# Performance work log

Hardware: AMD Instinct MI355X
Metric: run time of the kernel (lower is better)

Reference implementation:

```python
import jax, jax.numpy as jnp
import numpy as np

N, E, NFEAT, HID, HEADS, NCLASS = 100000, 1600000, 256, 64, 1, 32


def gat_conv(x, src, dst, W, a_src, a_dst, b, H, C, concat):
    n = x.shape[0]
    h = (x @ W).reshape(n, H, C)                      # [N,H,C]
    a_s = (h * a_src).sum(-1)                          # [N,H]
    a_d = (h * a_dst).sum(-1)                          # [N,H]
    e = jax.nn.leaky_relu(a_s[src] + a_d[dst], 0.2)    # [E,H]
    emax = jax.ops.segment_max(e, dst, num_segments=n)
    emax = jnp.where(jnp.isfinite(emax), emax, 0.0)
    ex = jnp.exp(e - emax[dst])
    denom = jax.ops.segment_sum(ex, dst, num_segments=n)
    alpha = ex / (denom[dst] + 1e-16)                  # segment softmax over in-edges of dst
    msg = h[src] * alpha[:, :, None]                   # [E,H,C]
    out = jax.ops.segment_sum(msg, dst, num_segments=n)
    out = out.reshape(n, H * C) if concat else out.mean(axis=1)
    return out + b


def setup_inputs() -> dict:
    key = jax.random.key(0)
    ks = jax.random.split(key, 14)
    x = jax.random.normal(ks[0], (N, NFEAT), dtype=jnp.float32)
    edge_index = jax.random.randint(ks[1], (2, E), 0, N, dtype=jnp.int64)
    s = 0.05
    return {
        'x': x, 'edge_index': edge_index,
        'W1': jax.random.normal(ks[2], (NFEAT, HEADS * HID), jnp.float32) * s,
        'as1': jax.random.normal(ks[3], (HEADS, HID), jnp.float32) * s,
        'ad1': jax.random.normal(ks[4], (HEADS, HID), jnp.float32) * s,
        'b1': jnp.zeros((HEADS * HID,), jnp.float32),
        'W2': jax.random.normal(ks[5], (HEADS * HID, HEADS * HID), jnp.float32) * s,
        'as2': jax.random.normal(ks[6], (HEADS, HID), jnp.float32) * s,
        'ad2': jax.random.normal(ks[7], (HEADS, HID), jnp.float32) * s,
        'b2': jnp.zeros((HEADS * HID,), jnp.float32),
        'W3': jax.random.normal(ks[8], (HEADS * HID, HEADS * NCLASS), jnp.float32) * s,
        'as3': jax.random.normal(ks[9], (HEADS, NCLASS), jnp.float32) * s,
        'ad3': jax.random.normal(ks[10], (HEADS, NCLASS), jnp.float32) * s,
        'b3': jnp.zeros((NCLASS,), jnp.float32),
    }


def reference(x, edge_index, W1, as1, ad1, b1, W2, as2, ad2, b2, W3, as3, ad3, b3):
    # add self loops (PyG GATConv add_self_loops=True)
    loop = jnp.arange(N, dtype=edge_index.dtype)
    src = jnp.concatenate([edge_index[0], loop])
    dst = jnp.concatenate([edge_index[1], loop])
    out = jax.nn.leaky_relu(gat_conv(x, src, dst, W1, as1, ad1, b1, HEADS, HID, True), 0.01)
    out = jax.nn.leaky_relu(gat_conv(out, src, dst, W2, as2, ad2, b2, HEADS, HID, True), 0.01)
    out = gat_conv(out, src, dst, W3, as3, ad3, b3, HEADS, NCLASS, False)
    return out
```

## Files before the change

kernel.cpp:

```cpp
#include <hip/hip_runtime.h>

#define NN 100000
#define NE 1600000
#define NF 256
#define HD 64
#define NC 32

#define BKS 8
#define NBK ((NN + 255) >> 8)
#define CHUNK 4096
#define NBLK ((NE + CHUNK - 1) / CHUNK)

__device__ __forceinline__ float lrelu02(float x) { return fmaxf(x, 0.2f * x); }

typedef __attribute__((ext_vector_type(8))) short bf16x8;
typedef __attribute__((ext_vector_type(4))) float f32x4;
typedef __attribute__((ext_vector_type(4))) _Float16 f16x4;

__device__ __forceinline__ unsigned short f2bf(float f) {
    unsigned int u = __float_as_uint(f);
    unsigned int r = u + 0x7FFFu + ((u >> 16) & 1u);
    return (unsigned short)(r >> 16);
}
__device__ __forceinline__ float bf2f(unsigned short s) {
    return __uint_as_float(((unsigned int)s) << 16);
}


__global__ __launch_bounds__(256) void bucket_hist(const int* __restrict__ dst, int* __restrict__ gcnt) {
    __shared__ int hist[NBK];
    int tid = threadIdx.x;
    for (int i = tid; i < NBK; i += 256) hist[i] = 0;
    __syncthreads();
    int base = blockIdx.x * CHUNK;
    #pragma unroll
    for (int k = 0; k < CHUNK / 256; k++) {
        int i = base + k * 256 + tid;
        if (i < NE) atomicAdd(&hist[dst[i] >> BKS], 1);
    }
    __syncthreads();
    for (int i = tid; i < NBK; i += 256) if (hist[i]) atomicAdd(&gcnt[i], hist[i]);
}

__global__ void bucket_scan(const int* __restrict__ gcnt, int* __restrict__ gbase, int* __restrict__ gcur) {
    __shared__ int sh[512];
    int tid = threadIdx.x;
    int v = (tid < NBK) ? gcnt[tid] : 0;
    sh[tid] = v;
    __syncthreads();
    for (int d = 1; d < 512; d <<= 1) {
        int t = (tid >= d) ? sh[tid - d] : 0;
        __syncthreads();
        sh[tid] += t;
        __syncthreads();
    }
    if (tid < NBK) { int ex = sh[tid] - v; gbase[tid] = ex; gcur[tid] = ex; }
}

__global__ __launch_bounds__(256) void bin_edges(const int* __restrict__ src, const int* __restrict__ dst,
                                                 int* __restrict__ gcur, int2* __restrict__ ebuf) {
    __shared__ int hist[NBK];
    __shared__ int excl[NBK];
    __shared__ int runbase[NBK];
    __shared__ int ssum[256];
    __shared__ int2 sorted[CHUNK];
    int tid = threadIdx.x;
    int base = blockIdx.x * CHUNK;
    int n = NE - base; if (n > CHUNK) n = CHUNK;

    for (int i = tid; i < NBK; i += 256) hist[i] = 0;
    __syncthreads();

    int2 ed[CHUNK / 256];
    int bk[CHUNK / 256];
    #pragma unroll
    for (int k = 0; k < CHUNK / 256; k++) {
        int i = base + k * 256 + tid;
        if (i < NE) {
            ed[k] = make_int2(src[i], dst[i]);
            bk[k] = ed[k].y >> BKS;
            atomicAdd(&hist[bk[k]], 1);
        } else bk[k] = -1;
    }
    __syncthreads();
    int h0 = (2 * tid < NBK) ? hist[2 * tid] : 0;
    int h1 = (2 * tid + 1 < NBK) ? hist[2 * tid + 1] : 0;
    ssum[tid] = h0 + h1;
    __syncthreads();
    for (int d = 1; d < 256; d <<= 1) {
        int t = (tid >= d) ? ssum[tid - d] : 0;
        __syncthreads();
        ssum[tid] += t;
        __syncthreads();
    }
    int pref = ssum[tid] - (h0 + h1);
    if (2 * tid < NBK) excl[2 * tid] = pref;
    if (2 * tid + 1 < NBK) excl[2 * tid + 1] = pref + h0;
    for (int b = tid; b < NBK; b += 256) {
        int c = hist[b];
        runbase[b] = c ? atomicAdd(&gcur[b], c) : 0;
    }
    __syncthreads();
    #pragma unroll
    for (int k = 0; k < CHUNK / 256; k++) {
        if (bk[k] >= 0) {
            int r = atomicAdd(&excl[bk[k]], 1);
            sorted[r] = ed[k];
        }
    }
    __syncthreads();
    for (int i = tid; i < n; i += 256) {
        int2 e = sorted[i];
        int b = e.y >> BKS;
        int local_rank = i - (excl[b] - hist[b]);
        ebuf[runbase[b] + local_rank] = e;
    }
}

__global__ __launch_bounds__(256) void bucket_csr(const int2* __restrict__ ebuf, const int* __restrict__ gbase,
                                                  const int* __restrict__ gcnt,
                                                  int* __restrict__ offs, int* __restrict__ csr) {
    __shared__ int hist[256], cur[256], ssum[256];
    int b = blockIdx.x, tid = threadIdx.x;
    int ebeg = gbase[b], cnt = gcnt[b];
    int node0 = b << BKS;
    hist[tid] = 0;
    __syncthreads();
    for (int i = ebeg + tid; i < ebeg + cnt; i += 256)
        atomicAdd(&hist[ebuf[i].y & 255], 1);
    __syncthreads();
    int v = hist[tid];
    ssum[tid] = v;
    __syncthreads();
    for (int d = 1; d < 256; d <<= 1) {
        int t = (tid >= d) ? ssum[tid - d] : 0;
        __syncthreads();
        ssum[tid] += t;
        __syncthreads();
    }
    int ex = ebeg + ssum[tid] - v;
    cur[tid] = ex;
    int nnode = NN - node0; if (nnode > 256) nnode = 256;
    if (tid < nnode) offs[node0 + tid] = ex;
    if (b == NBK - 1 && tid == nnode - 1) offs[NN] = ebeg + cnt;
    __syncthreads();
    for (int i = ebeg + tid; i < ebeg + cnt; i += 256) {
        int2 e = ebuf[i];
        int pos = atomicAdd(&cur[e.y & 255], 1);
        csr[pos] = e.x;
    }
}


template <int CIN, int COUT>
__global__ __launch_bounds__(128) void mfma_gemm(const float* __restrict__ in, const float* __restrict__ W,
                                                 const float* __restrict__ a_s, const float* __restrict__ a_d,
                                                 _Float16* __restrict__ hout, float* __restrict__ asv,
                                                 float* __restrict__ adv) {
    const int KC  = 32;
    const int BM  = 64;
    const int NCT = COUT / 16;
    const int NCH = CIN / KC;
    const int SPT = (4 * COUT) / 128;

    __shared__ unsigned short Bh[2][4 * COUT * 8];
    __shared__ unsigned short Bl[2][4 * COUT * 8];

    int tid  = threadIdx.x;
    int lane = tid & 63;
    int wave = tid >> 6;
    int fr = lane & 15;
    int kg = lane >> 4;
    int n0base = blockIdx.x * BM;
    int rbase  = n0base + wave * 32;

    int scol[SPT], skg[SPT];
    #pragma unroll
    for (int i = 0; i < SPT; i++) {
        int s = tid + i * 128;
        scol[i] = s % COUT;
        skg[i]  = s / COUT;
    }

    float4 xr[4];
    float  wv[SPT][8];
    bf16x8 ah[2], al[2];

    f32x4 acc[2][NCT];
    #pragma unroll
    for (int rt = 0; rt < 2; rt++)
        #pragma unroll
        for (int ct = 0; ct < NCT; ct++) acc[rt][ct] = (f32x4){0.f, 0.f, 0.f, 0.f};

    auto load_A = [&](int k0) {
        #pragma unroll
        for (int rt = 0; rt < 2; rt++) {
            int gr = rbase + rt * 16 + fr;
            if (gr < NN) {
                const float* p = &in[(size_t)gr * CIN + k0 + kg * 8];
                xr[rt * 2 + 0] = *(const float4*)p;
                xr[rt * 2 + 1] = *(const float4*)(p + 4);
            } else {
                xr[rt * 2 + 0] = make_float4(0.f, 0.f, 0.f, 0.f);
                xr[rt * 2 + 1] = make_float4(0.f, 0.f, 0.f, 0.f);
            }
        }
    };
    auto conv_A = [&]() {
        #pragma unroll
        for (int rt = 0; rt < 2; rt++) {
            const float* v = (const float*)&xr[rt * 2];
            unsigned short hs[8], ls[8];
            #pragma unroll
            for (int j = 0; j < 8; j++) {
                hs[j] = f2bf(v[j]);
                ls[j] = f2bf(v[j] - bf2f(hs[j]));
            }
            ah[rt] = *(bf16x8*)hs;
            al[rt] = *(bf16x8*)ls;
        }
    };
    auto load_B = [&](int k0) {
        #pragma unroll
        for (int i = 0; i < SPT; i++)
            #pragma unroll
            for (int j = 0; j < 8; j++)
                wv[i][j] = W[(size_t)(k0 + skg[i] * 8 + j) * COUT + scol[i]];
    };
    auto write_B = [&](int buf) {
        #pragma unroll
        for (int i = 0; i < SPT; i++) {
            unsigned short hs[8], ls[8];
            #pragma unroll
            for (int j = 0; j < 8; j++) {
                hs[j] = f2bf(wv[i][j]);
                ls[j] = f2bf(wv[i][j] - bf2f(hs[j]));
            }
            int idx = (skg[i] * COUT + scol[i]) * 8;
            *(uint4*)&Bh[buf][idx] = *(uint4*)hs;
            *(uint4*)&Bl[buf][idx] = *(uint4*)ls;
        }
    };
    auto do_mfma = [&](int buf) {
        #pragma unroll
        for (int ct = 0; ct < NCT; ct++) {
            int col = ct * 16 + fr;
            bf16x8 bh = *(const bf16x8*)&Bh[buf][(kg * COUT + col) * 8];
            bf16x8 bl = *(const bf16x8*)&Bl[buf][(kg * COUT + col) * 8];
            #pragma unroll
            for (int rt = 0; rt < 2; rt++) {
                acc[rt][ct] = __builtin_amdgcn_mfma_f32_16x16x32_bf16(ah[rt], bh, acc[rt][ct], 0, 0, 0);
                acc[rt][ct] = __builtin_amdgcn_mfma_f32_16x16x32_bf16(ah[rt], bl, acc[rt][ct], 0, 0, 0);
                acc[rt][ct] = __builtin_amdgcn_mfma_f32_16x16x32_bf16(al[rt], bh, acc[rt][ct], 0, 0, 0);
            }
        }
    };

    load_A(0);
    load_B(0);
    conv_A();
    write_B(0);
    __syncthreads();

    for (int t = 0; t < NCH; t++) {
        int cur = t & 1;
        if (t + 1 < NCH) {
            load_A((t + 1) * KC);
            load_B((t + 1) * KC);
        }
        do_mfma(cur);
        if (t + 1 < NCH) {
            write_B(cur ^ 1);
            conv_A();
            __syncthreads();
        }
    }

    float As_l[NCT], Ad_l[NCT];
    #pragma unroll
    for (int ct = 0; ct < NCT; ct++) {
        As_l[ct] = a_s[ct * 16 + fr];
        Ad_l[ct] = a_d[ct * 16 + fr];
    }
    #pragma unroll
    for (int rt = 0; rt < 2; rt++) {
        #pragma unroll
        for (int r = 0; r < 4; r++) {
            int row = rbase + rt * 16 + kg * 4 + r;
            if (row < NN) {
                #pragma unroll
                for (int ct = 0; ct < NCT; ct++)
                    hout[(size_t)row * COUT + ct * 16 + fr] = (_Float16)acc[rt][ct][r];
            }
            float ps = 0.f, pd = 0.f;
            #pragma unroll
            for (int ct = 0; ct < NCT; ct++) {
                ps += acc[rt][ct][r] * As_l[ct];
                pd += acc[rt][ct][r] * Ad_l[ct];
            }
            #pragma unroll
            for (int off = 1; off < 16; off <<= 1) {
                ps += __shfl_xor(ps, off);
                pd += __shfl_xor(pd, off);
            }
            if (fr == 0 && row < NN) { asv[row] = ps; adv[row] = pd; }
        }
    }
}


template <int C, bool ACT>
__global__ __launch_bounds__(256) void gat_agg(const _Float16* __restrict__ h16, const float* __restrict__ asv,
                                               const float* __restrict__ adv, const int* __restrict__ offs,
                                               const int* __restrict__ csr,
                                               const float* __restrict__ bias, float* __restrict__ out) {
    const int LPR = C / 4;
    const int G = 64 / LPR;
    const f16x4* hh = (const f16x4*)h16;
    int lane = threadIdx.x & 63;
    int v = blockIdx.x * 4 + (threadIdx.x >> 6);
    int beg = offs[v], end = offs[v + 1];
    int g = lane / LPR, r = lane % LPR;
    float adv_v = adv[v];

    float4 acc = {0.f, 0.f, 0.f, 0.f};
    float dsum = 0.f;
    #pragma unroll 4
    for (int e = beg + g; e < end; e += G) {
        int s = csr[e];
        float ww = __expf(lrelu02(asv[s] + adv_v));
        f16x4 hv = hh[(size_t)s * LPR + r];
        dsum += ww;
        acc.x += ww * (float)hv[0]; acc.y += ww * (float)hv[1];
        acc.z += ww * (float)hv[2]; acc.w += ww * (float)hv[3];
    }
    #pragma unroll
    for (int off = LPR; off < 64; off <<= 1) {
        acc.x += __shfl_xor(acc.x, off);
        acc.y += __shfl_xor(acc.y, off);
        acc.z += __shfl_xor(acc.z, off);
        acc.w += __shfl_xor(acc.w, off);
        dsum += __shfl_xor(dsum, off);
    }
    if (g == 0) {
        float selfw = __expf(lrelu02(asv[v] + adv_v));
        f16x4 hs = hh[(size_t)v * LPR + r];
        acc.x += selfw * (float)hs[0]; acc.y += selfw * (float)hs[1];
        acc.z += selfw * (float)hs[2]; acc.w += selfw * (float)hs[3];
        dsum += selfw;
        float inv = 1.f / (dsum + 1e-16f);
        float4 bb = ((const float4*)bias)[r];
        float4 o;
        o.x = acc.x * inv + bb.x; o.y = acc.y * inv + bb.y;
        o.z = acc.z * inv + bb.z; o.w = acc.w * inv + bb.w;
        if (ACT) {
            o.x = fmaxf(o.x, 0.01f * o.x); o.y = fmaxf(o.y, 0.01f * o.y);
            o.z = fmaxf(o.z, 0.01f * o.z); o.w = fmaxf(o.w, 0.01f * o.w);
        }
        ((float4*)out)[(size_t)v * LPR + r] = o;
    }
}


extern "C" void kernel_launch(void* const* d_in, const int* in_sizes, int n_in,
                              void* d_out, int out_size, void* d_ws, size_t ws_size,
                              hipStream_t stream) {
    const float* x   = (const float*)d_in[0];
    const int*   ei  = (const int*)d_in[1];
    const float* W1  = (const float*)d_in[2];
    const float* as1 = (const float*)d_in[3];
    const float* ad1 = (const float*)d_in[4];
    const float* b1  = (const float*)d_in[5];
    const float* W2  = (const float*)d_in[6];
    const float* as2 = (const float*)d_in[7];
    const float* ad2 = (const float*)d_in[8];
    const float* b2  = (const float*)d_in[9];
    const float* W3  = (const float*)d_in[10];
    const float* as3 = (const float*)d_in[11];
    const float* ad3 = (const float*)d_in[12];
    const float* b3  = (const float*)d_in[13];
    float* out = (float*)d_out;

    const int* srcp = ei;
    const int* dstp = ei + NE;

    char* w = (char*)d_ws;
    _Float16* h16 = (_Float16*)w;  w += sizeof(_Float16) * (size_t)NN * HD;
    float* featB = (float*)w;   w += sizeof(float) * (size_t)NN * HD;
    float* asv   = (float*)w;   w += sizeof(float) * NN;
    float* advv  = (float*)w;   w += sizeof(float) * NN;
    int* offs    = (int*)w;     w += sizeof(int) * (NN + 1);
    int* csr     = (int*)w;     w += sizeof(int) * (size_t)NE;
    int2* ebuf   = (int2*)w;    w += sizeof(int2) * (size_t)NE;
    int* gcnt    = (int*)w;     w += sizeof(int) * NBK;
    int* gbase   = (int*)w;     w += sizeof(int) * NBK;
    int* gcur    = (int*)w;     w += sizeof(int) * NBK;

    const int GBM = (NN + 63) / 64;

    hipMemsetAsync(gcnt, 0, sizeof(int) * NBK, stream);
    bucket_hist<<<NBLK, 256, 0, stream>>>(dstp, gcnt);
    bucket_scan<<<1, 512, 0, stream>>>(gcnt, gbase, gcur);
    bin_edges<<<NBLK, 256, 0, stream>>>(srcp, dstp, gcur, ebuf);
    bucket_csr<<<NBK, 256, 0, stream>>>(ebuf, gbase, gcnt, offs, csr);

    mfma_gemm<NF, HD><<<GBM, 128, 0, stream>>>(x, W1, as1, ad1, h16, asv, advv);
    gat_agg<HD, true><<<NN / 4, 256, 0, stream>>>(h16, asv, advv, offs, csr, b1, featB);

    mfma_gemm<HD, HD><<<GBM, 128, 0, stream>>>(featB, W2, as2, ad2, h16, asv, advv);
    gat_agg<HD, true><<<NN / 4, 256, 0, stream>>>(h16, asv, advv, offs, csr, b2, featB);

    mfma_gemm<HD, NC><<<GBM, 128, 0, stream>>>(featB, W3, as3, ad3, h16, asv, advv);
    gat_agg<NC, false><<<NN / 4, 256, 0, stream>>>(h16, asv, advv, offs, csr, b3, out);
}
```

Measured before the change: 427.6 us.

## Pack binned edges into 32-bit words and widen aggregation gathers to 8 halves

The binning pass now stores each edge as a single 32-bit word (source index shifted left by 8, plus the low 8 bits of the destination) instead of an int2, with a separate ushort shared array holding the bucket id. This halves the ebuf write and read traffic in bin_edges and bucket_csr. The aggregation kernel now loads 8 fp16 features per lane instead of 4, so each lane group covers a row in fewer lanes and more edges are processed in parallel per wavefront, at the cost of more accumulator registers. Packing works because source indices fit in 24 bits when N is 100000.

```diff
diff --git a/kernel.cpp b/kernel.cpp
--- a/kernel.cpp
+++ b/kernel.cpp
@@ -15,7 +15,7 @@
 
 typedef __attribute__((ext_vector_type(8))) short bf16x8;
 typedef __attribute__((ext_vector_type(4))) float f32x4;
-typedef __attribute__((ext_vector_type(4))) _Float16 f16x4;
+typedef __attribute__((ext_vector_type(8))) _Float16 f16x8;
 
 __device__ __forceinline__ unsigned short f2bf(float f) {
     unsigned int u = __float_as_uint(f);
@@ -58,12 +58,13 @@
 }
 
 __global__ __launch_bounds__(256) void bin_edges(const int* __restrict__ src, const int* __restrict__ dst,
-                                                 int* __restrict__ gcur, int2* __restrict__ ebuf) {
+                                                 int* __restrict__ gcur, unsigned int* __restrict__ ebuf) {
     __shared__ int hist[NBK];
     __shared__ int excl[NBK];
     __shared__ int runbase[NBK];
     __shared__ int ssum[256];
-    __shared__ int2 sorted[CHUNK];
+    __shared__ unsigned int sorted[CHUNK];
+    __shared__ unsigned short sortedb[CHUNK];
     int tid = threadIdx.x;
     int base = blockIdx.x * CHUNK;
     int n = NE - base; if (n > CHUNK) n = CHUNK;
@@ -71,14 +72,15 @@
     for (int i = tid; i < NBK; i += 256) hist[i] = 0;
     __syncthreads();
 
-    int2 ed[CHUNK / 256];
+    unsigned int pk[CHUNK / 256];
     int bk[CHUNK / 256];
     #pragma unroll
     for (int k = 0; k < CHUNK / 256; k++) {
         int i = base + k * 256 + tid;
         if (i < NE) {
-            ed[k] = make_int2(src[i], dst[i]);
-            bk[k] = ed[k].y >> BKS;
+            int s = src[i], d = dst[i];
+            pk[k] = ((unsigned int)s << 8) | ((unsigned int)d & 255u);
+            bk[k] = d >> BKS;
             atomicAdd(&hist[bk[k]], 1);
         } else bk[k] = -1;
     }
@@ -105,19 +107,19 @@
     for (int k = 0; k < CHUNK / 256; k++) {
         if (bk[k] >= 0) {
             int r = atomicAdd(&excl[bk[k]], 1);
-            sorted[r] = ed[k];
+            sorted[r] = pk[k];
+            sortedb[r] = (unsigned short)bk[k];
         }
     }
     __syncthreads();
     for (int i = tid; i < n; i += 256) {
-        int2 e = sorted[i];
-        int b = e.y >> BKS;
+        int b = sortedb[i];
         int local_rank = i - (excl[b] - hist[b]);
-        ebuf[runbase[b] + local_rank] = e;
-    }
-}
-
-__global__ __launch_bounds__(256) void bucket_csr(const int2* __restrict__ ebuf, const int* __restrict__ gbase,
+        ebuf[runbase[b] + local_rank] = sorted[i];
+    }
+}
+
+__global__ __launch_bounds__(256) void bucket_csr(const unsigned int* __restrict__ ebuf, const int* __restrict__ gbase,
                                                   const int* __restrict__ gcnt,
                                                   int* __restrict__ offs, int* __restrict__ csr) {
     __shared__ int hist[256], cur[256], ssum[256];
@@ -127,7 +129,7 @@
     hist[tid] = 0;
     __syncthreads();
     for (int i = ebeg + tid; i < ebeg + cnt; i += 256)
-        atomicAdd(&hist[ebuf[i].y & 255], 1);
+        atomicAdd(&hist[ebuf[i] & 255u], 1);
     __syncthreads();
     int v = hist[tid];
     ssum[tid] = v;
@@ -145,9 +147,9 @@
     if (b == NBK - 1 && tid == nnode - 1) offs[NN] = ebeg + cnt;
     __syncthreads();
     for (int i = ebeg + tid; i < ebeg + cnt; i += 256) {
-        int2 e = ebuf[i];
-        int pos = atomicAdd(&cur[e.y & 255], 1);
-        csr[pos] = e.x;
+        unsigned int e = ebuf[i];
+        int pos = atomicAdd(&cur[e & 255u], 1);
+        csr[pos] = (int)(e >> 8);
     }
 }
 
@@ -314,50 +316,54 @@
                                                const float* __restrict__ adv, const int* __restrict__ offs,
                                                const int* __restrict__ csr,
                                                const float* __restrict__ bias, float* __restrict__ out) {
-    const int LPR = C / 4;
-    const int G = 64 / LPR;
-    const f16x4* hh = (const f16x4*)h16;
+    const int LR = C / 8;
+    const int G  = 64 / LR;
+    const f16x8* hh = (const f16x8*)h16;
     int lane = threadIdx.x & 63;
     int v = blockIdx.x * 4 + (threadIdx.x >> 6);
     int beg = offs[v], end = offs[v + 1];
-    int g = lane / LPR, r = lane % LPR;
+    int g = lane / LR, r = lane % LR;
     float adv_v = adv[v];
 
-    float4 acc = {0.f, 0.f, 0.f, 0.f};
+    float acc[8] = {0.f, 0.f, 0.f, 0.f, 0.f, 0.f, 0.f, 0.f};
     float dsum = 0.f;
     #pragma unroll 4
     for (int e = beg + g; e < end; e += G) {
         int s = csr[e];
         float ww = __expf(lrelu02(asv[s] + adv_v));
-        f16x4 hv = hh[(size_t)s * LPR + r];
+        f16x8 hv = hh[(size_t)s * LR + r];
         dsum += ww;
-        acc.x += ww * (float)hv[0]; acc.y += ww * (float)hv[1];
-        acc.z += ww * (float)hv[2]; acc.w += ww * (float)hv[3];
-    }
-    #pragma unroll
-    for (int off = LPR; off < 64; off <<= 1) {
-        acc.x += __shfl_xor(acc.x, off);
-        acc.y += __shfl_xor(acc.y, off);
-        acc.z += __shfl_xor(acc.z, off);
-        acc.w += __shfl_xor(acc.w, off);
+        #pragma unroll
+        for (int j = 0; j < 8; j++) acc[j] += ww * (float)hv[j];
+    }
+    #pragma unroll
+    for (int off = LR; off < 64; off <<= 1) {
+        #pragma unroll
+        for (int j = 0; j < 8; j++) acc[j] += __shfl_xor(acc[j], off);
         dsum += __shfl_xor(dsum, off);
     }
     if (g == 0) {
         float selfw = __expf(lrelu02(asv[v] + adv_v));
-        f16x4 hs = hh[(size_t)v * LPR + r];
-        acc.x += selfw * (float)hs[0]; acc.y += selfw * (float)hs[1];
-        acc.z += selfw * (float)hs[2]; acc.w += selfw * (float)hs[3];
+        f16x8 hs = hh[(size_t)v * LR + r];
+        #pragma unroll
+        for (int j = 0; j < 8; j++) acc[j] += selfw * (float)hs[j];
         dsum += selfw;
         float inv = 1.f / (dsum + 1e-16f);
-        float4 bb = ((const float4*)bias)[r];
-        float4 o;
-        o.x = acc.x * inv + bb.x; o.y = acc.y * inv + bb.y;
-        o.z = acc.z * inv + bb.z; o.w = acc.w * inv + bb.w;
+        float4 bb0 = ((const float4*)bias)[r * 2];
+        float4 bb1 = ((const float4*)bias)[r * 2 + 1];
+        float4 o0, o1;
+        o0.x = acc[0] * inv + bb0.x; o0.y = acc[1] * inv + bb0.y;
+        o0.z = acc[2] * inv + bb0.z; o0.w = acc[3] * inv + bb0.w;
+        o1.x = acc[4] * inv + bb1.x; o1.y = acc[5] * inv + bb1.y;
+        o1.z = acc[6] * inv + bb1.z; o1.w = acc[7] * inv + bb1.w;
         if (ACT) {
-            o.x = fmaxf(o.x, 0.01f * o.x); o.y = fmaxf(o.y, 0.01f * o.y);
-            o.z = fmaxf(o.z, 0.01f * o.z); o.w = fmaxf(o.w, 0.01f * o.w);
-        }
-        ((float4*)out)[(size_t)v * LPR + r] = o;
+            o0.x = fmaxf(o0.x, 0.01f * o0.x); o0.y = fmaxf(o0.y, 0.01f * o0.y);
+            o0.z = fmaxf(o0.z, 0.01f * o0.z); o0.w = fmaxf(o0.w, 0.01f * o0.w);
+            o1.x = fmaxf(o1.x, 0.01f * o1.x); o1.y = fmaxf(o1.y, 0.01f * o1.y);
+            o1.z = fmaxf(o1.z, 0.01f * o1.z); o1.w = fmaxf(o1.w, 0.01f * o1.w);
+        }
+        ((float4*)out)[(size_t)v * (C / 4) + r * 2]     = o0;
+        ((float4*)out)[(size_t)v * (C / 4) + r * 2 + 1] = o1;
     }
 }
 
@@ -391,7 +397,7 @@
     float* advv  = (float*)w;   w += sizeof(float) * NN;
     int* offs    = (int*)w;     w += sizeof(int) * (NN + 1);
     int* csr     = (int*)w;     w += sizeof(int) * (size_t)NE;
-    int2* ebuf   = (int2*)w;    w += sizeof(int2) * (size_t)NE;
+    unsigned int* ebuf = (unsigned int*)w; w += sizeof(unsigned int) * (size_t)NE;
     int* gcnt    = (int*)w;     w += sizeof(int) * NBK;
     int* gbase   = (int*)w;     w += sizeof(int) * NBK;
     int* gcur    = (int*)w;     w += sizeof(int) * NBK;
```

Result: no change. 423.9 us (-0.9%).
